# Optimization experiments

Hardware: AMD Instinct MI355X
Metric: run time of the kernel (lower is better)

The kernel has to match this reference:

```python
import jax, jax.numpy as jnp
import numpy as np

B, H = 16384, 1024
EPS = 1e-5


def setup_inputs() -> dict:
    key = jax.random.key(0)
    ks = jax.random.split(key, 12)
    inp = {
        "t": 0,
        "h": jax.random.normal(ks[0], (B, H), jnp.float32),
        "e": jax.random.normal(ks[1], (B, H), jnp.float32),
        # LiquidNeuron params
        "W_rec": jax.random.normal(ks[2], (H, H), jnp.float32) * 0.1,
        "bias": jnp.zeros((H,), jnp.float32),
        "tau": jnp.ones((H,), jnp.float32),
        "decay": jnp.ones((H,), jnp.float32),
        "ln_w": jnp.ones((H,), jnp.float32),
        "ln_b": jnp.zeros((H,), jnp.float32),
        # context_encoder: Linear -> ReLU -> Linear (dropout = identity in eval)
        "ce_w1": jax.random.normal(ks[3], (H, H), jnp.float32) * (1.0 / np.sqrt(H)),
        "ce_b1": jnp.zeros((H,), jnp.float32),
        "ce_w2": jax.random.normal(ks[4], (H, H), jnp.float32) * (1.0 / np.sqrt(H)),
        "ce_b2": jnp.zeros((H,), jnp.float32),
        # param_modulator
        "pm_w": jax.random.normal(ks[5], (H, H), jnp.float32) * (1.0 / np.sqrt(H)),
        "pm_b": jnp.zeros((H,), jnp.float32),
    }
    return inp


def reference(t, h, e, W_rec, bias, tau, decay, ln_w, ln_b,
              ce_w1, ce_b1, ce_w2, ce_b2, pm_w, pm_b):
    # context encoder (eval mode: dropout is identity)
    context = jnp.maximum(h @ ce_w1.T + ce_b1, 0.0) @ ce_w2.T + ce_b2  # [B,H]
    pa = context @ pm_w.T + pm_b  # param_adjustment [B,H]
    # bmm(e[:,None,:], (W_rec*(1+pa)[:,:,None]).T) == (1+pa) * (e @ W_rec.T)
    matmul_result = (1.0 + pa) * (e @ W_rec.T)  # [B,H]
    tau_adjusted = tau * jax.nn.sigmoid(pa)  # [B,H]
    dh_dt = (-decay * h + matmul_result + bias) / tau_adjusted
    # LayerNorm over last dim
    mu = jnp.mean(dh_dt, axis=-1, keepdims=True)
    var = jnp.var(dh_dt, axis=-1, keepdims=True)
    dh_dt = (dh_dt - mu) * jax.lax.rsqrt(var + EPS) * ln_w + ln_b
    return dh_dt
```

## Files before the change

### kernel.cpp

```cpp
#include <hip/hip_runtime.h>
#include <stdint.h>

#define H_DIM 1024
#define B_DIM 16384

typedef unsigned short u16;
typedef short bf16x8 __attribute__((ext_vector_type(8)));
typedef unsigned short ushort8 __attribute__((ext_vector_type(8)));
typedef float f32x4 __attribute__((ext_vector_type(4)));

__device__ __forceinline__ u16 f2bf(float f) {
  union { float f; uint32_t u; } v; v.f = f;
  uint32_t r = v.u + 0x7fffu + ((v.u >> 16) & 1u);
  return (u16)(r >> 16);
}
__device__ __forceinline__ float bf2f(u16 x) {
  union { uint32_t u; float f; } v; v.u = ((uint32_t)x) << 16;
  return v.f;
}

#define GLDS16(gsrc, ldst)                                                                 \
  __builtin_amdgcn_global_load_lds((const __attribute__((address_space(1))) void*)(gsrc),  \
                                   (__attribute__((address_space(3))) void*)(ldst), 16, 0, 0)

__device__ __forceinline__ void cvt_region(const float* __restrict__ in, u16* __restrict__ out,
                                           int tid, int nthr, int ngroups) {
  const float4* in4 = (const float4*)in;
  ushort8* out8 = (ushort8*)out;
  for (int gi = tid; gi < ngroups; gi += nthr) {
    float4 a = in4[2 * gi];
    float4 b = in4[2 * gi + 1];
    ushort8 o;
    o[0] = f2bf(a.x); o[1] = f2bf(a.y); o[2] = f2bf(a.z); o[3] = f2bf(a.w);
    o[4] = f2bf(b.x); o[5] = f2bf(b.y); o[6] = f2bf(b.z); o[7] = f2bf(b.w);
    out8[gi] = o;
  }
}

__global__ __launch_bounds__(256) void cvt_all(const float* __restrict__ h,
                                               const float* __restrict__ e,
                                               const float* __restrict__ w1f,
                                               const float* __restrict__ pmwf,
                                               const float* __restrict__ wrecf,
                                               u16* __restrict__ hb, u16* __restrict__ eb,
                                               u16* __restrict__ o1, u16* __restrict__ o3,
                                               u16* __restrict__ o4,
                                               const float* __restrict__ tau,
                                               float* __restrict__ rtau) {
  const int b = blockIdx.x;
  const int BH8 = (B_DIM * H_DIM) / 8;
  const int HH8 = (H_DIM * H_DIM) / 8;
  if (b < 2048) {
    cvt_region(h, hb, b * 256 + threadIdx.x, 2048 * 256, BH8);
  } else if (b < 4096) {
    cvt_region(e, eb, (b - 2048) * 256 + threadIdx.x, 2048 * 256, BH8);
  } else if (b < 4352) {
    cvt_region(w1f, o1, (b - 4096) * 256 + threadIdx.x, 256 * 256, HH8);
  } else if (b < 4608) {
    cvt_region(pmwf, o3, (b - 4352) * 256 + threadIdx.x, 256 * 256, HH8);
  } else if (b < 4864) {
    cvt_region(wrecf, o4, (b - 4608) * 256 + threadIdx.x, 256 * 256, HH8);
  } else {
    for (int i = threadIdx.x; i < H_DIM; i += 256) rtau[i] = 1.0f / tau[i];
  }
}

__global__ __launch_bounds__(256) void tr_cvt_w2(const float* __restrict__ in,
                                                 u16* __restrict__ out) {
  __shared__ float tile[64][65];
  const int t = threadIdx.x;
  const int r0 = (blockIdx.x >> 4) * 64;
  const int c0 = (blockIdx.x & 15) * 64;
  const float4* in4 = (const float4*)in;
#pragma unroll
  for (int it = 0; it < 4; ++it) {
    const int idx = it * 256 + t;
    const int r = idx >> 4, c4 = idx & 15;
    float4 v = in4[(size_t)(r0 + r) * 256 + (c0 >> 2) + c4];
    tile[r][c4 * 4 + 0] = v.x; tile[r][c4 * 4 + 1] = v.y;
    tile[r][c4 * 4 + 2] = v.z; tile[r][c4 * 4 + 3] = v.w;
  }
  __syncthreads();
  ushort4* out4 = (ushort4*)out;
#pragma unroll
  for (int it = 0; it < 4; ++it) {
    const int idx = it * 256 + t;
    const int c = idx >> 4, r4 = idx & 15;
    ushort4 o;
    o.x = f2bf(tile[r4 * 4 + 0][c]); o.y = f2bf(tile[r4 * 4 + 1][c]);
    o.z = f2bf(tile[r4 * 4 + 2][c]); o.w = f2bf(tile[r4 * 4 + 3][c]);
    out4[(size_t)(c0 + c) * 256 + (r0 >> 2) + r4] = o;
  }
}

__global__ __launch_bounds__(256) void b32_prep(const float* __restrict__ pmw,
                                                const float* __restrict__ ceb2,
                                                const float* __restrict__ pmb,
                                                float* __restrict__ b32) {
  const int i = blockIdx.x * 256 + threadIdx.x;
  const float4* w4 = (const float4*)(pmw + (size_t)i * H_DIM);
  const float4* b4 = (const float4*)ceb2;
  float acc = pmb[i];
  for (int k = 0; k < 256; ++k) {
    float4 w = w4[k], b = b4[k];
    acc += w.x * b.x + w.y * b.y + w.z * b.z + w.w * b.w;
  }
  b32[i] = acc;
}

__global__ __launch_bounds__(256) void w32_gemm(const u16* __restrict__ A,
                                                const u16* __restrict__ Wt,
                                                u16* __restrict__ C) {
  const int t = threadIdx.x;
  const int wv = t >> 6, l = t & 63;
  const int l15 = l & 15, lg = l >> 4;
  const int m0 = (blockIdx.x >> 4) * 64 + (wv >> 1) * 32;
  const int n0 = (blockIdx.x & 15) * 64 + (wv & 1) * 32;

  const u16* ap0 = A + (size_t)(m0 + l15) * H_DIM + lg * 8;
  const u16* ap1 = ap0 + 16 * H_DIM;
  const u16* bp0 = Wt + (size_t)(n0 + l15) * H_DIM + lg * 8;
  const u16* bp1 = bp0 + 16 * H_DIM;

  f32x4 acc[2][2] = {};
#pragma unroll
  for (int kt = 0; kt < 32; ++kt) {
    bf16x8 aF[2], bF[2];
    aF[0] = *(const bf16x8*)(ap0 + kt * 32);
    aF[1] = *(const bf16x8*)(ap1 + kt * 32);
    bF[0] = *(const bf16x8*)(bp0 + kt * 32);
    bF[1] = *(const bf16x8*)(bp1 + kt * 32);
#pragma unroll
    for (int mi = 0; mi < 2; ++mi)
#pragma unroll
      for (int ni = 0; ni < 2; ++ni)
        acc[mi][ni] =
            __builtin_amdgcn_mfma_f32_16x16x32_bf16(aF[mi], bF[ni], acc[mi][ni], 0, 0, 0);
  }
#pragma unroll
  for (int mi = 0; mi < 2; ++mi)
#pragma unroll
    for (int ni = 0; ni < 2; ++ni) {
      const int col = n0 + ni * 16 + l15;
#pragma unroll
      for (int j = 0; j < 4; ++j) {
        const int row = m0 + mi * 16 + lg * 4 + j;
        C[(size_t)row * H_DIM + col] = f2bf(acc[mi][ni][j]);
      }
    }
}

template <int MODE>
__device__ __forceinline__ void subtile_step(u16* shp, int slot, int slot3, int aoff, int boff,
                                             int wv, const u16*& pA0, const u16*& pA1,
                                             const u16*& pB0, const u16*& pB1,
                                             f32x4 (&acc)[8][4]) {
  const u16* Ab = shp + slot * 16384 + aoff;
  const u16* Bb = shp + slot * 16384 + 8192 + boff;
  bf16x8 aF[8], bF[4];
#pragma unroll
  for (int i = 0; i < 4; ++i) aF[i] = *(const bf16x8*)(Ab + i * 512);
#pragma unroll
  for (int i = 0; i < 4; ++i) bF[i] = *(const bf16x8*)(Bb + i * 512);
#pragma unroll
  for (int i = 4; i < 8; ++i) aF[i] = *(const bf16x8*)(Ab + i * 512);
  if (MODE == 3) {
    u16* da = shp + slot3 * 16384 + wv * 1024;
    GLDS16(pA0, da); GLDS16(pA1, da + 512);
    u16* db = shp + slot3 * 16384 + 8192 + wv * 1024;
    GLDS16(pB0, db); GLDS16(pB1, db + 512);
    pA0 += 32; pA1 += 32; pB0 += 32; pB1 += 32;
  }
  __builtin_amdgcn_s_setprio(1);
#pragma unroll
  for (int mf = 0; mf < 4; ++mf)
#pragma unroll
    for (int nf = 0; nf < 4; ++nf)
      acc[mf][nf] = __builtin_amdgcn_mfma_f32_16x16x32_bf16(aF[mf], bF[nf], acc[mf][nf], 0, 0, 0);
#pragma unroll
  for (int mf = 4; mf < 8; ++mf)
#pragma unroll
    for (int nf = 0; nf < 4; ++nf)
      acc[mf][nf] = __builtin_amdgcn_mfma_f32_16x16x32_bf16(aF[mf], bF[nf], acc[mf][nf], 0, 0, 0);
  __builtin_amdgcn_s_setprio(0);
  if (MODE == 3) asm volatile("s_waitcnt vmcnt(8)" ::: "memory");
  if (MODE == 2) asm volatile("s_waitcnt vmcnt(4)" ::: "memory");
  if (MODE == 1) asm volatile("s_waitcnt vmcnt(0)" ::: "memory");
  __builtin_amdgcn_s_barrier();
}

template <bool RELU, bool HASBIAS, typename OUT>
__global__ __launch_bounds__(512, 2) void gemm256(const u16* __restrict__ A,
                                                  const u16* __restrict__ W,
                                                  const float* __restrict__ bias,
                                                  OUT* __restrict__ C) {
  extern __shared__ u16 sh[];
  const int t = threadIdx.x;
  const int wv = t >> 6, l = t & 63;
  const int wm = wv >> 2, wn = wv & 3;
  const int l15 = l & 15, lg = l >> 4;

  const int bid = blockIdx.x;
  const int logical = (bid & 7) * 32 + (bid >> 3);
  const int m0 = (logical >> 2) * 256;
  const int n0 = (logical & 3) * 256;

  const int koff = (lg ^ ((l15 >> 1) & 3)) * 8;
  const int aoff = (wm * 128 + l15) * 32 + koff;
  const int boff = (wn * 64 + l15) * 32 + koff;

  const int rowst = wv * 32 + (l >> 2);
  const int ksl = ((l & 3) ^ ((l >> 3) & 3)) * 8;
  const u16* pA0 = A + (size_t)(m0 + rowst) * H_DIM + ksl;
  const u16* pA1 = pA0 + 16 * H_DIM;
  const u16* pB0 = W + (size_t)(n0 + rowst) * H_DIM + ksl;
  const u16* pB1 = pB0 + 16 * H_DIM;

  f32x4 acc[8][4] = {};

#pragma unroll
  for (int s = 0; s < 3; ++s) {
    u16* da = sh + s * 16384 + wv * 1024;
    GLDS16(pA0, da); GLDS16(pA1, da + 512);
    u16* db = sh + s * 16384 + 8192 + wv * 1024;
    GLDS16(pB0, db); GLDS16(pB1, db + 512);
    pA0 += 32; pA1 += 32; pB0 += 32; pB1 += 32;
  }
  asm volatile("s_waitcnt vmcnt(8)" ::: "memory");
  __builtin_amdgcn_s_barrier();

  for (int s = 0; s < 29; ++s)
    subtile_step<3>(sh, s & 3, (s + 3) & 3, aoff, boff, wv, pA0, pA1, pB0, pB1, acc);
  subtile_step<2>(sh, 1, 0, aoff, boff, wv, pA0, pA1, pB0, pB1, acc);
  subtile_step<1>(sh, 2, 0, aoff, boff, wv, pA0, pA1, pB0, pB1, acc);
  subtile_step<0>(sh, 3, 0, aoff, boff, wv, pA0, pA1, pB0, pB1, acc);

  float bv[4];
#pragma unroll
  for (int nf = 0; nf < 4; ++nf)
    bv[nf] = HASBIAS ? bias[n0 + wn * 64 + nf * 16 + l15] : 0.0f;
#pragma unroll
  for (int mf = 0; mf < 8; ++mf) {
#pragma unroll
    for (int nf = 0; nf < 4; ++nf) {
      const int col = n0 + wn * 64 + nf * 16 + l15;
#pragma unroll
      for (int j = 0; j < 4; ++j) {
        const int row = m0 + wm * 128 + mf * 16 + lg * 4 + j;
        float v = acc[mf][nf][j] + bv[nf];
        if (RELU) v = fmaxf(v, 0.0f);
        if constexpr (sizeof(OUT) == 2)
          C[(size_t)row * H_DIM + col] = (OUT)f2bf(v);
        else
          C[(size_t)row * H_DIM + col] = v;
      }
    }
  }
}

__global__ __launch_bounds__(256) void liquid_ln(const u16* __restrict__ hb,
                                                 const u16* __restrict__ pa,
                                                 const u16* __restrict__ ev,
                                                 const float* __restrict__ bias,
                                                 const float* __restrict__ rtau,
                                                 const float* __restrict__ decay,
                                                 const float* __restrict__ lnw,
                                                 const float* __restrict__ lnb,
                                                 float* __restrict__ out) {
  const int wv = threadIdx.x >> 6, l = threadIdx.x & 63;
  const int row = blockIdx.x * 4 + wv;
  const size_t rb = (size_t)row * H_DIM;

  float d[16];
  float s = 0.f, ss = 0.f;
#pragma unroll
  for (int c = 0; c < 2; ++c) {
    const int col = c * 512 + l * 8;
    float b8[8], r8[8], dc8[8];
    *(float4*)b8 = *(const float4*)(bias + col);
    *(float4*)(b8 + 4) = *(const float4*)(bias + col + 4);
    *(float4*)r8 = *(const float4*)(rtau + col);
    *(float4*)(r8 + 4) = *(const float4*)(rtau + col + 4);
    *(float4*)dc8 = *(const float4*)(decay + col);
    *(float4*)(dc8 + 4) = *(const float4*)(decay + col + 4);
    ushort8 hv = *(const ushort8*)(hb + rb + col);
    ushort8 pv = *(const ushort8*)(pa + rb + col);
    ushort8 evv = *(const ushort8*)(ev + rb + col);
#pragma unroll
    for (int j = 0; j < 8; ++j) {
      const float hf = bf2f(hv[j]);
      const float p = bf2f(pv[j]);
      const float e = bf2f(evv[j]);
      const float num = fmaf(-dc8[j], hf, fmaf(1.0f + p, e, b8[j]));
      const float val = num * (1.0f + __expf(-p)) * r8[j];
      d[c * 8 + j] = val;
      s += val;
      ss += val * val;
    }
  }
#pragma unroll
  for (int off = 32; off; off >>= 1) {
    s += __shfl_xor(s, off);
    ss += __shfl_xor(ss, off);
  }
  const float mu = s * (1.0f / H_DIM);
  const float var = ss * (1.0f / H_DIM) - mu * mu;
  const float rstd = rsqrtf(var + 1e-5f);

#pragma unroll
  for (int c = 0; c < 2; ++c) {
    const int col = c * 512 + l * 8;
    float w8[8], lb8[8], o[8];
    *(float4*)w8 = *(const float4*)(lnw + col);
    *(float4*)(w8 + 4) = *(const float4*)(lnw + col + 4);
    *(float4*)lb8 = *(const float4*)(lnb + col);
    *(float4*)(lb8 + 4) = *(const float4*)(lnb + col + 4);
#pragma unroll
    for (int j = 0; j < 8; ++j) o[j] = fmaf((d[c * 8 + j] - mu) * rstd, w8[j], lb8[j]);
    *(float4*)(out + rb + col) = *(float4*)o;
    *(float4*)(out + rb + col + 4) = *(float4*)(o + 4);
  }
}

extern "C" void kernel_launch(void* const* d_in, const int* in_sizes, int n_in,
                              void* d_out, int out_size, void* d_ws, size_t ws_size,
                              hipStream_t stream) {
  const float* h = (const float*)d_in[1];
  const float* e = (const float*)d_in[2];
  const float* Wrec = (const float*)d_in[3];
  const float* bias = (const float*)d_in[4];
  const float* tau = (const float*)d_in[5];
  const float* decay = (const float*)d_in[6];
  const float* lnw = (const float*)d_in[7];
  const float* lnb = (const float*)d_in[8];
  const float* ce_w1 = (const float*)d_in[9];
  const float* ce_b1 = (const float*)d_in[10];
  const float* ce_w2 = (const float*)d_in[11];
  const float* ce_b2 = (const float*)d_in[12];
  const float* pm_w = (const float*)d_in[13];
  const float* pm_b = (const float*)d_in[14];
  float* out = (float*)d_out;

  char* ws = (char*)d_ws;
  const size_t MB = 1024 * 1024;
  u16* w1b = (u16*)(ws + 0 * MB);
  u16* w2t = (u16*)(ws + 2 * MB);
  u16* w3b = (u16*)(ws + 4 * MB);
  u16* w4b = (u16*)(ws + 6 * MB);
  u16* W32b = (u16*)(ws + 8 * MB);
  float* rtau = (float*)(ws + 10 * MB);
  float* b32 = (float*)(ws + 10 * MB + 8192);
  u16* hbf = (u16*)(ws + 12 * MB);
  u16* ebf = (u16*)(ws + 44 * MB);
  u16* t1 = (u16*)(ws + 76 * MB);
  u16* evb = (u16*)(ws + 76 * MB);
  u16* pab = (u16*)(ws + 108 * MB);

  cvt_all<<<4865, 256, 0, stream>>>(h, e, ce_w1, pm_w, Wrec, hbf, ebf, w1b, w3b, w4b, tau, rtau);
  tr_cvt_w2<<<256, 256, 0, stream>>>(ce_w2, w2t);
  b32_prep<<<4, 256, 0, stream>>>(pm_w, ce_b2, pm_b, b32);
  w32_gemm<<<256, 256, 0, stream>>>(w3b, w2t, W32b);

  const int LDS_BYTES = 131072;
  hipFuncSetAttribute((const void*)gemm256<true, true, u16>,
                      hipFuncAttributeMaxDynamicSharedMemorySize, LDS_BYTES);
  hipFuncSetAttribute((const void*)gemm256<false, true, u16>,
                      hipFuncAttributeMaxDynamicSharedMemorySize, LDS_BYTES);
  hipFuncSetAttribute((const void*)gemm256<false, false, u16>,
                      hipFuncAttributeMaxDynamicSharedMemorySize, LDS_BYTES);

  const int NWG = (B_DIM / 256) * (H_DIM / 256);
  gemm256<true, true, u16><<<NWG, 512, LDS_BYTES, stream>>>(hbf, w1b, ce_b1, t1);
  gemm256<false, true, u16><<<NWG, 512, LDS_BYTES, stream>>>(t1, W32b, b32, pab);
  gemm256<false, false, u16><<<NWG, 512, LDS_BYTES, stream>>>(ebf, w4b, nullptr, evb);

  liquid_ln<<<B_DIM / 4, 256, 0, stream>>>(hbf, pab, evb, bias, rtau, decay, lnw, lnb, out);
}
```

Baseline: 222.5 us.

## Fuse fp32-to-bf16 activation conversion into GEMM A-operand loads

Drops the separate pass that converted h and e to bf16. A new GEMM variant streams fp32 A tiles straight into LDS and converts them to bf16 in registers with packed cvt instructions before the MFMAs. The LayerNorm kernel now reads fp32 h directly. This removes a large read/write pass over two 16384x1024 tensors, but the GEMM moves twice the A bytes, uses more LDS (one workgroup per CU) and adds conversion ALU work in the inner loop.

Result: no change. 220.8 us (-0.8%).

```diff
diff --git a/kernel.cpp b/kernel.cpp
--- a/kernel.cpp
+++ b/kernel.cpp
@@ -17,6 +17,15 @@
 __device__ __forceinline__ float bf2f(u16 x) {
   union { uint32_t u; float f; } v; v.u = ((uint32_t)x) << 16;
   return v.f;
+}
+
+__device__ __forceinline__ bf16x8 cvt8(f32x4 a, f32x4 b) {
+  union { uint32_t u[4]; bf16x8 v; } r;
+  asm("v_cvt_pk_bf16_f32 %0, %1, %2" : "=v"(r.u[0]) : "v"(a[0]), "v"(a[1]));
+  asm("v_cvt_pk_bf16_f32 %0, %1, %2" : "=v"(r.u[1]) : "v"(a[2]), "v"(a[3]));
+  asm("v_cvt_pk_bf16_f32 %0, %1, %2" : "=v"(r.u[2]) : "v"(b[0]), "v"(b[1]));
+  asm("v_cvt_pk_bf16_f32 %0, %1, %2" : "=v"(r.u[3]) : "v"(b[2]), "v"(b[3]));
+  return r.v;
 }
 
 #define GLDS16(gsrc, ldst)                                                                 \
@@ -37,29 +46,21 @@
   }
 }
 
-__global__ __launch_bounds__(256) void cvt_all(const float* __restrict__ h,
-                                               const float* __restrict__ e,
-                                               const float* __restrict__ w1f,
-                                               const float* __restrict__ pmwf,
-                                               const float* __restrict__ wrecf,
-                                               u16* __restrict__ hb, u16* __restrict__ eb,
-                                               u16* __restrict__ o1, u16* __restrict__ o3,
-                                               u16* __restrict__ o4,
-                                               const float* __restrict__ tau,
-                                               float* __restrict__ rtau) {
+__global__ __launch_bounds__(256) void cvt_w(const float* __restrict__ w1f,
+                                             const float* __restrict__ pmwf,
+                                             const float* __restrict__ wrecf,
+                                             u16* __restrict__ o1, u16* __restrict__ o3,
+                                             u16* __restrict__ o4,
+                                             const float* __restrict__ tau,
+                                             float* __restrict__ rtau) {
   const int b = blockIdx.x;
-  const int BH8 = (B_DIM * H_DIM) / 8;
   const int HH8 = (H_DIM * H_DIM) / 8;
-  if (b < 2048) {
-    cvt_region(h, hb, b * 256 + threadIdx.x, 2048 * 256, BH8);
-  } else if (b < 4096) {
-    cvt_region(e, eb, (b - 2048) * 256 + threadIdx.x, 2048 * 256, BH8);
-  } else if (b < 4352) {
-    cvt_region(w1f, o1, (b - 4096) * 256 + threadIdx.x, 256 * 256, HH8);
-  } else if (b < 4608) {
-    cvt_region(pmwf, o3, (b - 4352) * 256 + threadIdx.x, 256 * 256, HH8);
-  } else if (b < 4864) {
-    cvt_region(wrecf, o4, (b - 4608) * 256 + threadIdx.x, 256 * 256, HH8);
+  if (b < 256) {
+    cvt_region(w1f, o1, b * 256 + threadIdx.x, 256 * 256, HH8);
+  } else if (b < 512) {
+    cvt_region(pmwf, o3, (b - 256) * 256 + threadIdx.x, 256 * 256, HH8);
+  } else if (b < 768) {
+    cvt_region(wrecf, o4, (b - 512) * 256 + threadIdx.x, 256 * 256, HH8);
   } else {
     for (int i = threadIdx.x; i < H_DIM; i += 256) rtau[i] = 1.0f / tau[i];
   }
@@ -173,12 +174,7 @@
   }
   __builtin_amdgcn_s_setprio(1);
 #pragma unroll
-  for (int mf = 0; mf < 4; ++mf)
-#pragma unroll
-    for (int nf = 0; nf < 4; ++nf)
-      acc[mf][nf] = __builtin_amdgcn_mfma_f32_16x16x32_bf16(aF[mf], bF[nf], acc[mf][nf], 0, 0, 0);
-#pragma unroll
-  for (int mf = 4; mf < 8; ++mf)
+  for (int mf = 0; mf < 8; ++mf)
 #pragma unroll
     for (int nf = 0; nf < 4; ++nf)
       acc[mf][nf] = __builtin_amdgcn_mfma_f32_16x16x32_bf16(aF[mf], bF[nf], acc[mf][nf], 0, 0, 0);
@@ -258,7 +254,113 @@
   }
 }
 
-__global__ __launch_bounds__(256) void liquid_ln(const u16* __restrict__ hb,
+template <int SLOT, int SLOT2, int MODE>
+__device__ __forceinline__ void sub_f32(u16* sh, int aoff0, int aoff1, int boff, int wv,
+                                        const float*& gA, const u16*& pB0, const u16*& pB1,
+                                        f32x4 (&acc)[8][4]) {
+  const char* Ab = (const char*)sh + SLOT * 32768;
+  const u16* Bb = sh + 49152 + SLOT * 8192 + boff;
+  bf16x8 aF[8], bF[4];
+#pragma unroll
+  for (int mf = 0; mf < 8; ++mf) {
+    f32x4 lo = *(const f32x4*)(Ab + aoff0 + mf * 2048);
+    f32x4 hi = *(const f32x4*)(Ab + aoff1 + mf * 2048);
+    aF[mf] = cvt8(lo, hi);
+  }
+#pragma unroll
+  for (int i = 0; i < 4; ++i) bF[i] = *(const bf16x8*)(Bb + i * 512);
+  if (MODE == 2) {
+#pragma unroll
+    for (int i = 0; i < 4; ++i)
+      GLDS16(gA + i * 8 * H_DIM, sh + SLOT2 * 16384 + (wv * 32 + i * 8) * 64);
+    gA += 32;
+    u16* db = sh + 49152 + SLOT2 * 8192 + wv * 1024;
+    GLDS16(pB0, db); GLDS16(pB1, db + 512);
+    pB0 += 32; pB1 += 32;
+  }
+  __builtin_amdgcn_s_setprio(1);
+#pragma unroll
+  for (int mf = 0; mf < 8; ++mf)
+#pragma unroll
+    for (int nf = 0; nf < 4; ++nf)
+      acc[mf][nf] = __builtin_amdgcn_mfma_f32_16x16x32_bf16(aF[mf], bF[nf], acc[mf][nf], 0, 0, 0);
+  __builtin_amdgcn_s_setprio(0);
+  if (MODE == 2) asm volatile("s_waitcnt vmcnt(6)" ::: "memory");
+  if (MODE == 1) asm volatile("s_waitcnt vmcnt(0)" ::: "memory");
+  __builtin_amdgcn_s_barrier();
+}
+
+template <bool RELU, bool HASBIAS>
+__global__ __launch_bounds__(512, 1) void gemm256_f32a(const float* __restrict__ A,
+                                                       const u16* __restrict__ W,
+                                                       const float* __restrict__ bias,
+                                                       u16* __restrict__ C) {
+  extern __shared__ u16 sh[];
+  const int t = threadIdx.x;
+  const int wv = t >> 6, l = t & 63;
+  const int wm = wv >> 2, wn = wv & 3;
+  const int l15 = l & 15, lg = l >> 4;
+
+  const int bid = blockIdx.x;
+  const int logical = (bid & 7) * 32 + (bid >> 3);
+  const int m0 = (logical >> 2) * 256;
+  const int n0 = (logical & 3) * 256;
+
+  const int arow = (wm * 128 + l15) * 128;
+  const int aoff0 = arow + (((lg << 1) | 0) ^ (l15 & 7)) * 16;
+  const int aoff1 = arow + (((lg << 1) | 1) ^ (l15 & 7)) * 16;
+  const int boff = (wn * 64 + l15) * 32 + (lg ^ ((l15 >> 1) & 3)) * 8;
+
+  const float* gA = A + (size_t)(m0 + wv * 32 + (l >> 3)) * H_DIM + (((l & 7) ^ ((l >> 3) & 7)) << 2);
+  const int rowst = wv * 32 + (l >> 2);
+  const int ksl = ((l & 3) ^ ((l >> 3) & 3)) * 8;
+  const u16* pB0 = W + (size_t)(n0 + rowst) * H_DIM + ksl;
+  const u16* pB1 = pB0 + 16 * H_DIM;
+
+  f32x4 acc[8][4] = {};
+
+#pragma unroll
+  for (int s = 0; s < 2; ++s) {
+#pragma unroll
+    for (int i = 0; i < 4; ++i)
+      GLDS16(gA + i * 8 * H_DIM, sh + s * 16384 + (wv * 32 + i * 8) * 64);
+    gA += 32;
+    u16* db = sh + 49152 + s * 8192 + wv * 1024;
+    GLDS16(pB0, db); GLDS16(pB1, db + 512);
+    pB0 += 32; pB1 += 32;
+  }
+  asm volatile("s_waitcnt vmcnt(6)" ::: "memory");
+  __builtin_amdgcn_s_barrier();
+
+  for (int su = 0; su < 10; ++su) {
+    sub_f32<0, 2, 2>(sh, aoff0, aoff1, boff, wv, gA, pB0, pB1, acc);
+    sub_f32<1, 0, 2>(sh, aoff0, aoff1, boff, wv, gA, pB0, pB1, acc);
+    sub_f32<2, 1, 2>(sh, aoff0, aoff1, boff, wv, gA, pB0, pB1, acc);
+  }
+  sub_f32<0, 0, 1>(sh, aoff0, aoff1, boff, wv, gA, pB0, pB1, acc);
+  sub_f32<1, 0, 0>(sh, aoff0, aoff1, boff, wv, gA, pB0, pB1, acc);
+
+  float bv[4];
+#pragma unroll
+  for (int nf = 0; nf < 4; ++nf)
+    bv[nf] = HASBIAS ? bias[n0 + wn * 64 + nf * 16 + l15] : 0.0f;
+#pragma unroll
+  for (int mf = 0; mf < 8; ++mf) {
+#pragma unroll
+    for (int nf = 0; nf < 4; ++nf) {
+      const int col = n0 + wn * 64 + nf * 16 + l15;
+#pragma unroll
+      for (int j = 0; j < 4; ++j) {
+        const int row = m0 + wm * 128 + mf * 16 + lg * 4 + j;
+        float v = acc[mf][nf][j] + bv[nf];
+        if (RELU) v = fmaxf(v, 0.0f);
+        C[(size_t)row * H_DIM + col] = f2bf(v);
+      }
+    }
+  }
+}
+
+__global__ __launch_bounds__(256) void liquid_ln(const float* __restrict__ h,
                                                  const u16* __restrict__ pa,
                                                  const u16* __restrict__ ev,
                                                  const float* __restrict__ bias,
@@ -276,22 +378,22 @@
 #pragma unroll
   for (int c = 0; c < 2; ++c) {
     const int col = c * 512 + l * 8;
-    float b8[8], r8[8], dc8[8];
+    float h8[8], b8[8], r8[8], dc8[8];
+    *(float4*)h8 = *(const float4*)(h + rb + col);
+    *(float4*)(h8 + 4) = *(const float4*)(h + rb + col + 4);
     *(float4*)b8 = *(const float4*)(bias + col);
     *(float4*)(b8 + 4) = *(const float4*)(bias + col + 4);
     *(float4*)r8 = *(const float4*)(rtau + col);
     *(float4*)(r8 + 4) = *(const float4*)(rtau + col + 4);
     *(float4*)dc8 = *(const float4*)(decay + col);
     *(float4*)(dc8 + 4) = *(const float4*)(decay + col + 4);
-    ushort8 hv = *(const ushort8*)(hb + rb + col);
     ushort8 pv = *(const ushort8*)(pa + rb + col);
     ushort8 evv = *(const ushort8*)(ev + rb + col);
 #pragma unroll
     for (int j = 0; j < 8; ++j) {
-      const float hf = bf2f(hv[j]);
       const float p = bf2f(pv[j]);
       const float e = bf2f(evv[j]);
-      const float num = fmaf(-dc8[j], hf, fmaf(1.0f + p, e, b8[j]));
+      const float num = fmaf(-dc8[j], h8[j], fmaf(1.0f + p, e, b8[j]));
       const float val = num * (1.0f + __expf(-p)) * r8[j];
       d[c * 8 + j] = val;
       s += val;
@@ -350,29 +452,28 @@
   u16* W32b = (u16*)(ws + 8 * MB);
   float* rtau = (float*)(ws + 10 * MB);
   float* b32 = (float*)(ws + 10 * MB + 8192);
-  u16* hbf = (u16*)(ws + 12 * MB);
-  u16* ebf = (u16*)(ws + 44 * MB);
-  u16* t1 = (u16*)(ws + 76 * MB);
+  u16* t1 = (u16*)(ws + 12 * MB);
+  u16* pab = (u16*)(ws + 44 * MB);
   u16* evb = (u16*)(ws + 76 * MB);
-  u16* pab = (u16*)(ws + 108 * MB);
-
-  cvt_all<<<4865, 256, 0, stream>>>(h, e, ce_w1, pm_w, Wrec, hbf, ebf, w1b, w3b, w4b, tau, rtau);
+
+  cvt_w<<<769, 256, 0, stream>>>(ce_w1, pm_w, Wrec, w1b, w3b, w4b, tau, rtau);
   tr_cvt_w2<<<256, 256, 0, stream>>>(ce_w2, w2t);
   b32_prep<<<4, 256, 0, stream>>>(pm_w, ce_b2, pm_b, b32);
   w32_gemm<<<256, 256, 0, stream>>>(w3b, w2t, W32b);
 
-  const int LDS_BYTES = 131072;
-  hipFuncSetAttribute((const void*)gemm256<true, true, u16>,
-                      hipFuncAttributeMaxDynamicSharedMemorySize, LDS_BYTES);
+  const int LDS_BF16 = 131072;
+  const int LDS_F32 = 147456;
+  hipFuncSetAttribute((const void*)gemm256_f32a<true, true>,
+                      hipFuncAttributeMaxDynamicSharedMemorySize, LDS_F32);
+  hipFuncSetAttribute((const void*)gemm256_f32a<false, false>,
+                      hipFuncAttributeMaxDynamicSharedMemorySize, LDS_F32);
   hipFuncSetAttribute((const void*)gemm256<false, true, u16>,
-                      hipFuncAttributeMaxDynamicSharedMemorySize, LDS_BYTES);
-  hipFuncSetAttribute((const void*)gemm256<false, false, u16>,
-                      hipFuncAttributeMaxDynamicSharedMemorySize, LDS_BYTES);
+                      hipFuncAttributeMaxDynamicSharedMemorySize, LDS_BF16);
 
   const int NWG = (B_DIM / 256) * (H_DIM / 256);
-  gemm256<true, true, u16><<<NWG, 512, LDS_BYTES, stream>>>(hbf, w1b, ce_b1, t1);
-  gemm256<false, true, u16><<<NWG, 512, LDS_BYTES, stream>>>(t1, W32b, b32, pab);
-  gemm256<false, false, u16><<<NWG, 512, LDS_BYTES, stream>>>(ebf, w4b, nullptr, evb);
-
-  liquid_ln<<<B_DIM / 4, 256, 0, stream>>>(hbf, pab, evb, bias, rtau, decay, lnw, lnb, out);
-}
+  gemm256_f32a<true, true><<<NWG, 512, LDS_F32, stream>>>(h, w1b, ce_b1, t1);
+  gemm256<false, true, u16><<<NWG, 512, LDS_BF16, stream>>>(t1, W32b, b32, pab);
+  gemm256_f32a<false, false><<<NWG, 512, LDS_F32, stream>>>(e, w4b, nullptr, evb);
+
+  liquid_ln<<<B_DIM / 4, 256, 0, stream>>>(h, pab, evb, bias, rtau, decay, lnw, lnb, out);
+}
```
